# Performance work log

Measured on AMD Instinct MI355X. Metric: run time of the kernel, lower is better.

Reference implementation:

```python
import jax, jax.numpy as jnp
import numpy as np

N = 100_000      # nodes
DEG = 16         # avg in-degree (fixed per node for setup)
E = N * DEG      # edges
IN = 256         # in_feats
H = 4            # num_heads
D = 64           # out_feats per head
NEG_SLOPE = 0.2


def setup_inputs() -> dict:
    key = jax.random.key(0)
    k1, k2, k3, k4, k5 = jax.random.split(key, 5)
    # dst-major CSR with uniform degree DEG per destination node
    row_ptr = jnp.arange(N + 1, dtype=jnp.int32) * DEG          # [N+1]
    col_ind = jax.random.randint(k1, (E,), 0, N, dtype=jnp.int32)  # source ids per edge
    feat = jax.random.normal(k2, (N, IN), dtype=jnp.float32)
    # fc.weight (xavier-ish scale), torch Linear: y = x @ W.T
    W = jax.random.normal(k3, (H * D, IN), dtype=jnp.float32) * (1.0 / np.sqrt(IN))
    attn_l = jax.random.normal(k4, (1, H, D), dtype=jnp.float32) * 0.1
    attn_r = jax.random.normal(k5, (1, H, D), dtype=jnp.float32) * 0.1
    return {"row_ptr": row_ptr, "col_ind": col_ind, "feat": feat,
            "W": W, "attn_l": attn_l, "attn_r": attn_r}


def reference(row_ptr, col_ind, feat, W, attn_l, attn_r):
    n_nodes = feat.shape[0]
    n_edges = col_ind.shape[0]
    # feat_src = feat_dst = fc(feat).view(-1, H, D)
    feat_src = (feat @ W.T).reshape(n_nodes, H, D)
    el = jnp.sum(feat_src * attn_l, axis=-1)   # [N, H]
    er = jnp.sum(feat_src * attn_r, axis=-1)   # [N, H]
    # per-edge dst id from CSR row_ptr; src = col_ind
    dst = (jnp.searchsorted(row_ptr, jnp.arange(n_edges, dtype=row_ptr.dtype),
                            side='right') - 1).astype(jnp.int32)
    src = col_ind
    # e = u_add_v(g, er, el) -> er[src] + el[dst], then LeakyReLU
    e = er[src] + el[dst]                      # [E, H]
    e = jnp.where(e > 0, e, NEG_SLOPE * e)
    # CSR edge-softmax: normalize over incoming edges of each dst row
    m = jax.ops.segment_max(e, dst, num_segments=n_nodes)    # [N, H]
    ex = jnp.exp(e - m[dst])
    s = jax.ops.segment_sum(ex, dst, num_segments=n_nodes)   # [N, H]
    a = ex / s[dst]                                          # [E, H]
    # multi-head SpMM: out[n,h] = sum_{e: dst=n} a[e,h] * feat_src[src[e],h]
    outs = []
    for h in range(H):  # small fixed head loop to avoid [E,H,D] intermediate
        msg = a[:, h, None] * feat_src[src, h]               # [E, D]
        outs.append(jax.ops.segment_sum(msg, dst, num_segments=n_nodes))
    return jnp.stack(outs, axis=1)                           # [N, H, D]
```

## Files before the change

### kernel.cpp

```cpp
#include <hip/hip_runtime.h>
#include <math.h>


#define HEADS 4
#define KIN 256
#define NOUT 256
#define NEG_SLOPE 0.2f

typedef __attribute__((ext_vector_type(4))) short short4v;
typedef __attribute__((ext_vector_type(8))) short short8v;
typedef __attribute__((ext_vector_type(4))) float floatx4;

static __device__ __forceinline__ unsigned short f2bf(float x) {
  unsigned u = __float_as_uint(x);
  u += 0x7FFFu + ((u >> 16) & 1u);
  return (unsigned short)(u >> 16);
}
static __device__ __forceinline__ float bf2f(unsigned short b) {
  return __uint_as_float(((unsigned)b) << 16);
}

__global__ __launch_bounds__(256) void k_cast_w(const float* __restrict__ W,
                                                unsigned short* __restrict__ Wbf) {
  const int i = blockIdx.x * 256 + threadIdx.x;
  float4 f = ((const float4*)W)[i];
  ushort4 o;
  o.x = f2bf(f.x); o.y = f2bf(f.y); o.z = f2bf(f.z); o.w = f2bf(f.w);
  ((ushort4*)Wbf)[i] = o;
}

__global__ __launch_bounds__(256, 2) void k_gemm_mfma(
    const float* __restrict__ feat, const unsigned short* __restrict__ Wbf,
    const float* __restrict__ attn_l, const float* __restrict__ attn_r,
    unsigned short* __restrict__ fs_h, float* __restrict__ el_h,
    float* __restrict__ er_h, int n_nodes) {
  __shared__ unsigned short Alds[2][64 * 64];

  const int tid = threadIdx.x;
  const int lane = tid & 63;
  const int w = tid >> 6;
  const int m0 = blockIdx.x * 64;
  const int q = lane >> 4;
  const int l15 = lane & 15;

  floatx4 acc[4][4];
#pragma unroll
  for (int mt = 0; mt < 4; ++mt)
#pragma unroll
    for (int nt = 0; nt < 4; ++nt)
#pragma unroll
      for (int r = 0; r < 4; ++r) acc[mt][nt][r] = 0.0f;

  const int ar = tid >> 2;
  const int aj = tid & 3;
  const int r7 = ar & 7;
  int agr = m0 + ar;
  if (agr >= n_nodes) agr = n_nodes - 1;
  const float* __restrict__ abase = feat + (size_t)agr * KIN + aj * 16;
  unsigned short* const aw0 = &Alds[0][ar * 64 + ((2 * aj + 0) ^ r7) * 8];
  unsigned short* const aw1 = &Alds[0][ar * 64 + ((2 * aj + 1) ^ r7) * 8];
  const int bufoff = 64 * 64;

  float4 rg[2][4];

#pragma unroll
  for (int i = 0; i < 4; ++i) rg[0][i] = *(const float4*)(abase + i * 4);

#pragma unroll
  for (int kc = 0; kc < 4; ++kc) {
    const int b = kc & 1;
    {
      const float4* R = rg[b];
      short8v g0, g1;
      g0[0] = (short)f2bf(R[0].x); g0[1] = (short)f2bf(R[0].y);
      g0[2] = (short)f2bf(R[0].z); g0[3] = (short)f2bf(R[0].w);
      g0[4] = (short)f2bf(R[1].x); g0[5] = (short)f2bf(R[1].y);
      g0[6] = (short)f2bf(R[1].z); g0[7] = (short)f2bf(R[1].w);
      g1[0] = (short)f2bf(R[2].x); g1[1] = (short)f2bf(R[2].y);
      g1[2] = (short)f2bf(R[2].z); g1[3] = (short)f2bf(R[2].w);
      g1[4] = (short)f2bf(R[3].x); g1[5] = (short)f2bf(R[3].y);
      g1[6] = (short)f2bf(R[3].z); g1[7] = (short)f2bf(R[3].w);
      *(short8v*)(aw0 + b * bufoff) = g0;
      *(short8v*)(aw1 + b * bufoff) = g1;
    }
    if (kc < 3) {
      const float* p = abase + (kc + 1) * 64;
#pragma unroll
      for (int i = 0; i < 4; ++i) rg[(kc + 1) & 1][i] = *(const float4*)(p + i * 4);
    }
    __syncthreads();

    short8v bfr[2][4];
#pragma unroll
    for (int ks = 0; ks < 2; ++ks)
#pragma unroll
      for (int nt = 0; nt < 4; ++nt)
        bfr[ks][nt] = *(const short8v*)(Wbf + (size_t)(w * 64 + nt * 16 + l15) * KIN +
                                        kc * 64 + ks * 32 + q * 8);

#pragma unroll
    for (int ks = 0; ks < 2; ++ks) {
      short8v af[4];
#pragma unroll
      for (int mt = 0; mt < 4; ++mt) {
        const int slot = (ks * 4 + q) ^ (l15 & 7);
        af[mt] = *(const short8v*)(&Alds[b][(mt * 16 + l15) * 64 + slot * 8]);
      }
#pragma unroll
      for (int mt = 0; mt < 4; ++mt)
#pragma unroll
        for (int nt = 0; nt < 4; ++nt)
          acc[mt][nt] = __builtin_amdgcn_mfma_f32_16x16x32_bf16(
              af[mt], bfr[ks][nt], acc[mt][nt], 0, 0, 0);
    }
  }

  float alv[4], arv[4];
#pragma unroll
  for (int nt = 0; nt < 4; ++nt) {
    alv[nt] = attn_l[w * 64 + nt * 16 + l15];
    arv[nt] = attn_r[w * 64 + nt * 16 + l15];
  }
#pragma unroll
  for (int mt = 0; mt < 4; ++mt) {
#pragma unroll
    for (int r = 0; r < 4; ++r) {
      const int m = m0 + mt * 16 + q * 4 + r;
      const bool mvalid = (m < n_nodes);
      float pl = 0.f, pr = 0.f;
#pragma unroll
      for (int nt = 0; nt < 4; ++nt) {
        const float v = acc[mt][nt][r];
        pl = fmaf(v, alv[nt], pl);
        pr = fmaf(v, arv[nt], pr);
        if (mvalid)
          fs_h[((size_t)w * n_nodes + m) * 64 + nt * 16 + l15] = f2bf(v);
      }
#pragma unroll
      for (int off = 1; off < 16; off <<= 1) {
        pl += __shfl_xor(pl, off, 64);
        pr += __shfl_xor(pr, off, 64);
      }
      if (l15 == 0 && mvalid) {
        el_h[(size_t)w * n_nodes + m] = pl;
        er_h[(size_t)w * n_nodes + m] = pr;
      }
    }
  }
}

__global__ __launch_bounds__(256, 4) void k_aggregate(
    const int* __restrict__ row_ptr, const int* __restrict__ col_ind,
    const float* __restrict__ el_h, const float* __restrict__ er_h,
    const unsigned short* __restrict__ fs_h, float* __restrict__ out,
    int n_nodes) {
  const int bid = blockIdx.x;
  const int lane = threadIdx.x & 63;
  const int w = threadIdx.x >> 6;
  const int x = bid & 7;
  const int h = x >> 1;
  const int idx = (bid >> 3) * 2 + (x & 1);
  const int node = idx * 4 + w;
  if (node >= n_nodes) return;

  const int j = lane & 15;
  const int rs = row_ptr[node];
  const int deg = row_ptr[node + 1] - rs;
  const bool valid = (j < deg);
  const int src = valid ? col_ind[rs + j] : 0;

  const size_t hN = (size_t)h * n_nodes;
  float e = valid ? (er_h[hN + src] + el_h[hN + node]) : -INFINITY;
  e = (e > 0.f) ? e : NEG_SLOPE * e;

  float mx = e;
#pragma unroll
  for (int off = 1; off < 16; off <<= 1) mx = fmaxf(mx, __shfl_xor(mx, off, 64));
  float ex = valid ? __expf(e - mx) : 0.f;
  float s = ex;
#pragma unroll
  for (int off = 1; off < 16; off <<= 1) s += __shfl_xor(s, off, 64);
  const float a = ex / s;

  const int e8 = lane >> 3;
  const int c = lane & 7;
  const int s0 = __shfl(src, e8, 64);
  const int s1 = __shfl(src, 8 + e8, 64);
  const float w0 = __shfl(a, e8, 64);
  const float w1 = __shfl(a, 8 + e8, 64);
  const uint4 u0 = ((const uint4*)(fs_h + (hN + (size_t)s0) * 64))[c];
  const uint4 u1 = ((const uint4*)(fs_h + (hN + (size_t)s1) * 64))[c];

  float acc[8];
#pragma unroll
  for (int k = 0; k < 8; ++k) acc[k] = 0.f;
  acc[0] = fmaf(w0, __uint_as_float(u0.x << 16), acc[0]);
  acc[1] = fmaf(w0, __uint_as_float(u0.x & 0xFFFF0000u), acc[1]);
  acc[2] = fmaf(w0, __uint_as_float(u0.y << 16), acc[2]);
  acc[3] = fmaf(w0, __uint_as_float(u0.y & 0xFFFF0000u), acc[3]);
  acc[4] = fmaf(w0, __uint_as_float(u0.z << 16), acc[4]);
  acc[5] = fmaf(w0, __uint_as_float(u0.z & 0xFFFF0000u), acc[5]);
  acc[6] = fmaf(w0, __uint_as_float(u0.w << 16), acc[6]);
  acc[7] = fmaf(w0, __uint_as_float(u0.w & 0xFFFF0000u), acc[7]);
  acc[0] = fmaf(w1, __uint_as_float(u1.x << 16), acc[0]);
  acc[1] = fmaf(w1, __uint_as_float(u1.x & 0xFFFF0000u), acc[1]);
  acc[2] = fmaf(w1, __uint_as_float(u1.y << 16), acc[2]);
  acc[3] = fmaf(w1, __uint_as_float(u1.y & 0xFFFF0000u), acc[3]);
  acc[4] = fmaf(w1, __uint_as_float(u1.z << 16), acc[4]);
  acc[5] = fmaf(w1, __uint_as_float(u1.z & 0xFFFF0000u), acc[5]);
  acc[6] = fmaf(w1, __uint_as_float(u1.w << 16), acc[6]);
  acc[7] = fmaf(w1, __uint_as_float(u1.w & 0xFFFF0000u), acc[7]);

#pragma unroll
  for (int off = 8; off < 64; off <<= 1)
#pragma unroll
    for (int k = 0; k < 8; ++k) acc[k] += __shfl_xor(acc[k], off, 64);

  if (lane < 8) {
    float* op = out + ((size_t)node * HEADS + h) * 64 + lane * 8;
    *(float4*)op = make_float4(acc[0], acc[1], acc[2], acc[3]);
    *(float4*)(op + 4) = make_float4(acc[4], acc[5], acc[6], acc[7]);
  }
}

extern "C" void kernel_launch(void* const* d_in, const int* in_sizes, int n_in,
                              void* d_out, int out_size, void* d_ws, size_t ws_size,
                              hipStream_t stream) {
  const int* row_ptr = (const int*)d_in[0];
  const int* col_ind = (const int*)d_in[1];
  const float* feat = (const float*)d_in[2];
  const float* W = (const float*)d_in[3];
  const float* attn_l = (const float*)d_in[4];
  const float* attn_r = (const float*)d_in[5];
  float* out = (float*)d_out;
  const int n_nodes = in_sizes[0] - 1;

  char* ws = (char*)d_ws;
  unsigned short* Wbf = (unsigned short*)ws;
  unsigned short* fs_h = (unsigned short*)(ws + 128 * 1024);
  size_t fs_bytes = (size_t)n_nodes * NOUT * sizeof(unsigned short);
  float* el_h = (float*)(ws + 128 * 1024 + fs_bytes);
  float* er_h = el_h + (size_t)n_nodes * HEADS;

  k_cast_w<<<64, 256, 0, stream>>>(W, Wbf);
  k_gemm_mfma<<<(n_nodes + 63) / 64, 256, 0, stream>>>(
      feat, Wbf, attn_l, attn_r, fs_h, el_h, er_h, n_nodes);

  int nb_per_head = (n_nodes + 3) / 4;
  nb_per_head += (nb_per_head & 1);
  k_aggregate<<<nb_per_head * 4, 256, 0, stream>>>(
      row_ptr, col_ind, el_h, er_h, fs_h, out, n_nodes);
}
```

Measured before the change: 380.5 us.

## Process four destination nodes per wavefront in aggregate kernel

The aggregation kernel now maps four destination nodes to each 64-lane wavefront, 16 lanes per node, instead of one node per wave that left 48 lanes idle during the softmax phase. The gather phase issues eight independent 128-bit loads per lane, which raises memory-level parallelism, and the grid shrinks fourfold. In exchange it uses more registers for four accumulator sets and adds shuffle-reduction work that could lower occupancy. Correctness relies on each node having a degree of at most 16.

```diff
diff --git a/kernel.cpp b/kernel.cpp
--- a/kernel.cpp
+++ b/kernel.cpp
@@ -160,17 +160,19 @@
   const int x = bid & 7;
   const int h = x >> 1;
   const int idx = (bid >> 3) * 2 + (x & 1);
-  const int node = idx * 4 + w;
-  if (node >= n_nodes) return;
-
+  const int nbase = idx * 16 + w * 4;
+
+  const int g = lane >> 4;
   const int j = lane & 15;
-  const int rs = row_ptr[node];
-  const int deg = row_ptr[node + 1] - rs;
-  const bool valid = (j < deg);
+  const int node = nbase + g;
+  const int nclamp = (node < n_nodes) ? node : (n_nodes - 1);
+  const int rs = row_ptr[nclamp];
+  const int deg = row_ptr[nclamp + 1] - rs;
+  const bool valid = (node < n_nodes) && (j < deg);
   const int src = valid ? col_ind[rs + j] : 0;
 
   const size_t hN = (size_t)h * n_nodes;
-  float e = valid ? (er_h[hN + src] + el_h[hN + node]) : -INFINITY;
+  float e = valid ? (er_h[hN + src] + el_h[hN + nclamp]) : -INFINITY;
   e = (e > 0.f) ? e : NEG_SLOPE * e;
 
   float mx = e;
@@ -184,42 +186,69 @@
 
   const int e8 = lane >> 3;
   const int c = lane & 7;
-  const int s0 = __shfl(src, e8, 64);
-  const int s1 = __shfl(src, 8 + e8, 64);
-  const float w0 = __shfl(a, e8, 64);
-  const float w1 = __shfl(a, 8 + e8, 64);
-  const uint4 u0 = ((const uint4*)(fs_h + (hN + (size_t)s0) * 64))[c];
-  const uint4 u1 = ((const uint4*)(fs_h + (hN + (size_t)s1) * 64))[c];
-
-  float acc[8];
-#pragma unroll
-  for (int k = 0; k < 8; ++k) acc[k] = 0.f;
-  acc[0] = fmaf(w0, __uint_as_float(u0.x << 16), acc[0]);
-  acc[1] = fmaf(w0, __uint_as_float(u0.x & 0xFFFF0000u), acc[1]);
-  acc[2] = fmaf(w0, __uint_as_float(u0.y << 16), acc[2]);
-  acc[3] = fmaf(w0, __uint_as_float(u0.y & 0xFFFF0000u), acc[3]);
-  acc[4] = fmaf(w0, __uint_as_float(u0.z << 16), acc[4]);
-  acc[5] = fmaf(w0, __uint_as_float(u0.z & 0xFFFF0000u), acc[5]);
-  acc[6] = fmaf(w0, __uint_as_float(u0.w << 16), acc[6]);
-  acc[7] = fmaf(w0, __uint_as_float(u0.w & 0xFFFF0000u), acc[7]);
-  acc[0] = fmaf(w1, __uint_as_float(u1.x << 16), acc[0]);
-  acc[1] = fmaf(w1, __uint_as_float(u1.x & 0xFFFF0000u), acc[1]);
-  acc[2] = fmaf(w1, __uint_as_float(u1.y << 16), acc[2]);
-  acc[3] = fmaf(w1, __uint_as_float(u1.y & 0xFFFF0000u), acc[3]);
-  acc[4] = fmaf(w1, __uint_as_float(u1.z << 16), acc[4]);
-  acc[5] = fmaf(w1, __uint_as_float(u1.z & 0xFFFF0000u), acc[5]);
-  acc[6] = fmaf(w1, __uint_as_float(u1.w << 16), acc[6]);
-  acc[7] = fmaf(w1, __uint_as_float(u1.w & 0xFFFF0000u), acc[7]);
-
-#pragma unroll
-  for (int off = 8; off < 64; off <<= 1)
-#pragma unroll
-    for (int k = 0; k < 8; ++k) acc[k] += __shfl_xor(acc[k], off, 64);
-
-  if (lane < 8) {
-    float* op = out + ((size_t)node * HEADS + h) * 64 + lane * 8;
-    *(float4*)op = make_float4(acc[0], acc[1], acc[2], acc[3]);
-    *(float4*)(op + 4) = make_float4(acc[4], acc[5], acc[6], acc[7]);
+
+  int sj[8];
+#pragma unroll
+  for (int p = 0; p < 8; ++p) sj[p] = __shfl(src, p * 8 + e8, 64);
+
+  uint4 u[8];
+#pragma unroll
+  for (int p = 0; p < 8; ++p)
+    u[p] = ((const uint4*)(fs_h + (hN + (size_t)sj[p]) * 64))[c];
+
+  float wgt[8];
+#pragma unroll
+  for (int p = 0; p < 8; ++p) wgt[p] = __shfl(a, p * 8 + e8, 64);
+
+  float ac0[8], ac1[8], ac2[8], ac3[8];
+#pragma unroll
+  for (int k = 0; k < 8; ++k) { ac0[k] = 0.f; ac1[k] = 0.f; ac2[k] = 0.f; ac3[k] = 0.f; }
+
+#define ACCUM(A, p)                                          \
+  do {                                                       \
+    const uint4 v = u[p];                                    \
+    const float w0 = wgt[p];                                 \
+    A[0] = fmaf(w0, __uint_as_float(v.x << 16), A[0]);       \
+    A[1] = fmaf(w0, __uint_as_float(v.x & 0xFFFF0000u), A[1]); \
+    A[2] = fmaf(w0, __uint_as_float(v.y << 16), A[2]);       \
+    A[3] = fmaf(w0, __uint_as_float(v.y & 0xFFFF0000u), A[3]); \
+    A[4] = fmaf(w0, __uint_as_float(v.z << 16), A[4]);       \
+    A[5] = fmaf(w0, __uint_as_float(v.z & 0xFFFF0000u), A[5]); \
+    A[6] = fmaf(w0, __uint_as_float(v.w << 16), A[6]);       \
+    A[7] = fmaf(w0, __uint_as_float(v.w & 0xFFFF0000u), A[7]); \
+  } while (0)
+
+  ACCUM(ac0, 0); ACCUM(ac0, 1);
+  ACCUM(ac1, 2); ACCUM(ac1, 3);
+  ACCUM(ac2, 4); ACCUM(ac2, 5);
+  ACCUM(ac3, 6); ACCUM(ac3, 7);
+#undef ACCUM
+
+#pragma unroll
+  for (int off = 8; off < 64; off <<= 1) {
+#pragma unroll
+    for (int k = 0; k < 8; ++k) {
+      ac0[k] += __shfl_xor(ac0[k], off, 64);
+      ac1[k] += __shfl_xor(ac1[k], off, 64);
+      ac2[k] += __shfl_xor(ac2[k], off, 64);
+      ac3[k] += __shfl_xor(ac3[k], off, 64);
+    }
+  }
+
+  if (lane < 32) {
+    const int sg = lane >> 3;
+    const int sc = lane & 7;
+    const int sn = nbase + sg;
+    if (sn < n_nodes) {
+      float v[8];
+#pragma unroll
+      for (int k = 0; k < 8; ++k)
+        v[k] = (sg & 2) ? ((sg & 1) ? ac3[k] : ac2[k])
+                        : ((sg & 1) ? ac1[k] : ac0[k]);
+      float* op = out + ((size_t)sn * HEADS + h) * 64 + sc * 8;
+      *(float4*)op = make_float4(v[0], v[1], v[2], v[3]);
+      *(float4*)(op + 4) = make_float4(v[4], v[5], v[6], v[7]);
+    }
   }
 }
 
@@ -246,8 +275,8 @@
   k_gemm_mfma<<<(n_nodes + 63) / 64, 256, 0, stream>>>(
       feat, Wbf, attn_l, attn_r, fs_h, el_h, er_h, n_nodes);
 
-  int nb_per_head = (n_nodes + 3) / 4;
-  nb_per_head += (nb_per_head & 1);
-  k_aggregate<<<nb_per_head * 4, 256, 0, stream>>>(
+  int nb16 = (n_nodes + 15) / 16;
+  nb16 += (nb16 & 1);
+  k_aggregate<<<nb16 * 4, 256, 0, stream>>>(
       row_ptr, col_ind, el_h, er_h, fs_h, out, n_nodes);
 }
```

Measured after the change: 340.6 us. -10.5%, faster.
